# Kernel tuning notes

Hardware: AMD Instinct MI355X
Metric: run time of the kernel (lower is better)

Reference implementation:

```python
import jax, jax.numpy as jnp
import numpy as np

KERNEL_MUL = 2.0
KERNEL_NUM = 5
FIX_SIGMA = None


def setup_inputs() -> dict:
    key = jax.random.key(0)
    k1, k2 = jax.random.split(key)
    B, N, D = 4, 2048, 64
    return {
        "input": jax.random.normal(k1, (B, N, D), dtype=jnp.float32),
        "target": jax.random.normal(k2, (B, N, D), dtype=jnp.float32),
    }


def _mmd(x, y):
    B = x.shape[0]
    x = x.reshape(B, -1, x.shape[-1])
    y = y.reshape(B, -1, y.shape[-1])
    n = x.shape[1]
    total = jnp.concatenate([x, y], axis=1)          # [B, N, D], N = n + m
    N = total.shape[1]
    # pairwise squared L2 via |a|^2 + |b|^2 - 2 a.b (avoids [B,N,N,D] tensor)
    sq = jnp.sum(total * total, axis=-1)             # [B, N]
    gram = jnp.einsum('bnd,bmd->bnm', total, total)  # [B, N, N]
    L2 = sq[:, :, None] + sq[:, None, :] - 2.0 * gram
    if FIX_SIGMA is not None:
        bandwidth = jnp.full((B,), FIX_SIGMA, dtype=L2.dtype)
    else:
        bandwidth = jnp.sum(jax.lax.stop_gradient(L2), axis=(-1, -2)) / (N * N - N)
    bandwidth = bandwidth / (KERNEL_MUL ** (KERNEL_NUM // 2))   # [B]
    # multi-bandwidth Gaussian kernel sum (small fixed loop over KERNEL_NUM)
    kernels = jnp.zeros_like(L2)
    for i in range(KERNEL_NUM):
        bw_i = bandwidth * (KERNEL_MUL ** i)          # [B]
        kernels = kernels + jnp.exp(-L2 / bw_i[:, None, None])
    XX = kernels[:, :n, :n]
    YY = kernels[:, n:, n:]
    XY = kernels[:, :n, n:]
    YX = kernels[:, n:, :n]
    loss = (XX + YY - XY - YX).reshape(B, -1).mean(axis=-1)  # [B]
    return loss


def reference(input, target):
    return _mmd(input, target)
```

## Files before the change

kernel.cpp:

```cpp
#include <hip/hip_runtime.h>

#define N_TOT 4096
#define N_HALF 2048
#define DIMS 64
#define BATCH 4
#define WGRID 64
#define TRI_PER_BATCH 2080
#define NWG (BATCH * TRI_PER_BATCH)

typedef __attribute__((ext_vector_type(8))) short short8;
typedef __attribute__((ext_vector_type(4))) float f32x4;

#if __has_builtin(__builtin_amdgcn_exp2f)
#define EXP2F(x) __builtin_amdgcn_exp2f(x)
#else
#define EXP2F(x) exp2f(x)
#endif

__device__ __forceinline__ unsigned short f2bf_rne(float f) {
    unsigned int u = __float_as_uint(f);
    unsigned int r = (u + 0x7FFFu + ((u >> 16) & 1u)) >> 16;
    return (unsigned short)r;
}
__device__ __forceinline__ float bf2f(unsigned short h) {
    return __uint_as_float(((unsigned int)h) << 16);
}

__global__ __launch_bounds__(256) void prep_kernel(const float* __restrict__ x,
                                                   const float* __restrict__ y,
                                                   unsigned short* __restrict__ hi,
                                                   unsigned short* __restrict__ lo,
                                                   float* __restrict__ sq,
                                                   float* __restrict__ ssq_part,
                                                   float* __restrict__ colsum_part) {
    int g = blockIdx.x;
    int t = threadIdx.x;
    bool isx = g < 128;
    int gg = isx ? g : g - 128;
    int base = gg << 12;
    int b = gg >> 5;
    const float* src = isx ? x : y;

    float q_acc = 0.f;
    float4 c_acc = {0.f, 0.f, 0.f, 0.f};
#pragma unroll
    for (int it = 0; it < 4; ++it) {
        int e = base + (it << 10) + (t << 2);
        int rem = e & 131071;
        float4 v = *(const float4*)(src + e);
        unsigned dst = (unsigned)b * 262144u + (isx ? 0u : 131072u) + (unsigned)rem;
        ushort4 h, l;
        h.x = f2bf_rne(v.x); l.x = f2bf_rne(v.x - bf2f(h.x));
        h.y = f2bf_rne(v.y); l.y = f2bf_rne(v.y - bf2f(h.y));
        h.z = f2bf_rne(v.z); l.z = f2bf_rne(v.z - bf2f(h.z));
        h.w = f2bf_rne(v.w); l.w = f2bf_rne(v.w - bf2f(h.w));
        *(ushort4*)(hi + dst) = h;
        *(ushort4*)(lo + dst) = l;

        float p = fmaf(v.x, v.x, fmaf(v.y, v.y, fmaf(v.z, v.z, v.w * v.w)));
        p += __shfl_xor(p, 1);
        p += __shfl_xor(p, 2);
        p += __shfl_xor(p, 4);
        p += __shfl_xor(p, 8);
        int rwi = rem >> 6;
        if ((t & 15) == 0)
            sq[b * N_TOT + (isx ? rwi : N_HALF + rwi)] = p;

        float q = p;
        q += __shfl_xor(q, 16);
        q += __shfl_xor(q, 32);
        q_acc += q;

        float4 c = v;
        c.x += __shfl_xor(c.x, 16); c.y += __shfl_xor(c.y, 16);
        c.z += __shfl_xor(c.z, 16); c.w += __shfl_xor(c.w, 16);
        c.x += __shfl_xor(c.x, 32); c.y += __shfl_xor(c.y, 32);
        c.z += __shfl_xor(c.z, 32); c.w += __shfl_xor(c.w, 32);
        c_acc.x += c.x; c_acc.y += c.y; c_acc.z += c.z; c_acc.w += c.w;
    }

    __shared__ float wsum[4];
    __shared__ float4 csh[4][16];
    int wid = t >> 6;
    if ((t & 63) == 0) wsum[wid] = q_acc;
    if ((t & 63) < 16) csh[wid][t & 63] = c_acc;
    __syncthreads();
    if (t == 0) ssq_part[g] = wsum[0] + wsum[1] + wsum[2] + wsum[3];
    if (t < 16) {
        float4 s0 = csh[0][t], s1 = csh[1][t], s2 = csh[2][t], s3 = csh[3][t];
        float4 o;
        o.x = s0.x + s1.x + s2.x + s3.x;
        o.y = s0.y + s1.y + s2.y + s3.y;
        o.z = s0.z + s1.z + s2.z + s3.z;
        o.w = s0.w + s1.w + s2.w + s3.w;
        *(float4*)(colsum_part + (size_t)g * 64 + t * 4) = o;
    }
}

__global__ __launch_bounds__(256) void bw_kernel(const float* __restrict__ ssq_part,
                                                 const float* __restrict__ colsum_part,
                                                 float* __restrict__ k0arr) {
    int b = blockIdx.x;
    int t = threadIdx.x;
    int c = t & 63, q = t >> 6;
    float cs = 0.f;
#pragma unroll
    for (int pp = 0; pp < 16; ++pp) {
        int p = q * 16 + pp;
        int g = (p < 32) ? (b * 32 + p) : (128 + b * 32 + (p - 32));
        cs += colsum_part[(size_t)g * 64 + c];
    }
    __shared__ float csq[4][64];
    csq[q][c] = cs;
    __syncthreads();
    if (t < 64) {
        float col = csq[0][t] + csq[1][t] + csq[2][t] + csq[3][t];
        double cc = (double)col * (double)col;
#pragma unroll
        for (int o = 32; o > 0; o >>= 1) cc += __shfl_xor(cc, o);
        int g = (t < 32) ? (b * 32 + t) : (128 + b * 32 + (t - 32));
        double sd = (double)ssq_part[g];
#pragma unroll
        for (int o = 32; o > 0; o >>= 1) sd += __shfl_xor(sd, o);
        if (t == 0) {
            double sumL2 = 2.0 * (double)N_TOT * sd - 2.0 * cc;
            double bw = sumL2 / ((double)N_TOT * (double)N_TOT - (double)N_TOT);
            bw *= 0.25;
            k0arr[b] = (float)(-1.4426950408889634 / bw);
        }
    }
}

#define MMD_TILE_BODY(DIAGW)                                                   \
    _Pragma("unroll")                                                          \
    for (int mf = 0; mf < 4; ++mf) {                                           \
        unsigned ra = (i0 + (unsigned)mf * 16u + lrow) * 64u + kbase;          \
        short8 ah0 = *(const short8*)(Hb + ra);                                \
        short8 ah1 = *(const short8*)(Hb + ra + 32u);                          \
        short8 al0 = *(const short8*)(Lb + ra);                                \
        short8 al1 = *(const short8*)(Lb + ra + 32u);                          \
        float4 sv = *(const float4*)(sqb + i0 + (unsigned)mf * 16u + rquad);   \
        float ki0 = k16 * sv.x, ki1 = k16 * sv.y;                              \
        float ki2 = k16 * sv.z, ki3 = k16 * sv.w;                              \
        _Pragma("unroll")                                                      \
        for (int nf = 0; nf < 4; ++nf) {                                       \
            const short* bp = B0 + (nf * 16 + (int)lrow) * 8;                  \
            short8 bh0 = *(const short8*)(bp);                                 \
            short8 bh1 = *(const short8*)(bp + 2048);                          \
            f32x4 accP = (f32x4){0.f, 0.f, 0.f, 0.f};                          \
            f32x4 accQ = (f32x4){0.f, 0.f, 0.f, 0.f};                          \
            accP = __builtin_amdgcn_mfma_f32_16x16x32_bf16(ah0, bh0, accP, 0, 0, 0); \
            accQ = __builtin_amdgcn_mfma_f32_16x16x32_bf16(ah1, bh1, accQ, 0, 0, 0); \
            accP = __builtin_amdgcn_mfma_f32_16x16x32_bf16(al0, bh0, accP, 0, 0, 0); \
            accQ = __builtin_amdgcn_mfma_f32_16x16x32_bf16(al1, bh1, accQ, 0, 0, 0); \
            float kjn = (nf == 0) ? kj0 : (nf == 1) ? kj1 : (nf == 2) ? kj2 : kj3; \
            _Pragma("unroll")                                                  \
            for (int rg = 0; rg < 4; ++rg) {                                   \
                float kir = (rg == 0) ? ki0 : (rg == 1) ? ki1 : (rg == 2) ? ki2 : ki3; \
                float t16 = fmaf(m2k16, accQ[rg], fmaf(m2k16, accP[rg], kir + kjn)); \
                float e4 = EXP2F(t16);                                         \
                float e3 = e4 * e4;                                            \
                float e2 = e3 * e3;                                            \
                float e1 = e2 * e2;                                            \
                float e0 = e1 * e1;                                            \
                float es = ((e0 + e1) + (e2 + e3)) + e4;                       \
                if (DIAGW) {                                                   \
                    int i = mf * 16 + (int)rquad + rg;                         \
                    int j = nf * 16 + (int)lrow;                               \
                    float w = (j > i) ? 2.f : ((j == i) ? 1.f : 0.f);          \
                    es *= w;                                                   \
                }                                                              \
                if (rg & 1) eacc1 += es; else eacc0 += es;                     \
            }                                                                  \
        }                                                                      \
    }

__global__ void mmd_mfma(const unsigned short* __restrict__ hi,
                         const unsigned short* __restrict__ lo,
                         const float* __restrict__ sq,
                         const float* __restrict__ k0arr,
                         double* __restrict__ pblock) {
    int wg0 = blockIdx.x;
    int wg = (wg0 & 7) * (NWG / 8) + (wg0 >> 3);
    int b = wg / TRI_PER_BATCH;
    int r = wg % TRI_PER_BATCH;
    int ib = 0, cum = 0;
    while (r >= cum + (WGRID - ib)) { cum += WGRID - ib; ++ib; }
    int jb = ib + (r - cum);
    unsigned i0 = (unsigned)ib * 64u;
    unsigned j0 = (unsigned)jb * 64u;
    int lane = threadIdx.x;

    const unsigned short* Hb = hi + (unsigned)b * 262144u;
    const unsigned short* Lb = lo + (unsigned)b * 262144u;
    const float* sqb = sq + b * N_TOT;

    __shared__ short ldsB[4096];
    {
        unsigned gb = (j0 + (unsigned)lane) * 64u;
#pragma unroll
        for (int k = 0; k < 8; ++k) {
            short8 v = *(const short8*)(Hb + gb + (unsigned)k * 8u);
            *(short8*)(ldsB + k * 512 + lane * 8) = v;
        }
    }

    bool diag = (ib == jb);
    float wsign = ((i0 < (unsigned)N_HALF) == (j0 < (unsigned)N_HALF)) ? 1.f : -1.f;
    float k16 = k0arr[b] * 0.0625f;
    float m2k16 = -2.f * k16;
    unsigned lrow = (unsigned)(lane & 15);
    unsigned grp = (unsigned)(lane >> 4);
    unsigned rquad = grp * 4u;
    unsigned kbase = grp * 8u;

    float kj0 = k16 * sqb[j0 + 0u + lrow];
    float kj1 = k16 * sqb[j0 + 16u + lrow];
    float kj2 = k16 * sqb[j0 + 32u + lrow];
    float kj3 = k16 * sqb[j0 + 48u + lrow];

    const short* B0 = ldsB + grp * 512;
    float eacc0 = 0.f, eacc1 = 0.f;

    if (diag) {
        MMD_TILE_BODY(true)
    } else {
        MMD_TILE_BODY(false)
    }

    double acc_d = (double)((eacc0 + eacc1) * (diag ? wsign : 2.f * wsign));
#pragma unroll
    for (int o = 32; o > 0; o >>= 1) acc_d += __shfl_down(acc_d, o);
    if (lane == 0) pblock[wg] = acc_d;
}

__global__ __launch_bounds__(256) void finalize_kernel(const double* __restrict__ pblock,
                                                       float* __restrict__ out) {
    int b = blockIdx.x, t = threadIdx.x;
    const double* p = pblock + (size_t)b * TRI_PER_BATCH;
    double s = 0.0;
    for (int i = t; i < TRI_PER_BATCH; i += 256) s += p[i];
#pragma unroll
    for (int o = 32; o > 0; o >>= 1) s += __shfl_down(s, o);
    __shared__ double w[4];
    if ((t & 63) == 0) w[t >> 6] = s;
    __syncthreads();
    if (t == 0)
        out[b] = (float)((w[0] + w[1] + w[2] + w[3]) / ((double)N_HALF * (double)N_HALF));
}

extern "C" void kernel_launch(void* const* d_in, const int* in_sizes, int n_in,
                              void* d_out, int out_size, void* d_ws, size_t ws_size,
                              hipStream_t stream) {
    const float* x = (const float*)d_in[0];
    const float* y = (const float*)d_in[1];
    float* out = (float*)d_out;
    char* ws = (char*)d_ws;

    float*  k0arr       = (float*)ws;
    float*  ssq_part    = (float*)(ws + 4096);
    float*  colsum_part = (float*)(ws + 8192);
    double* pblock      = (double*)(ws + 8192);
    float*  sq          = (float*)(ws + 77824);
    unsigned short* tot_hi = (unsigned short*)(ws + 143360);
    unsigned short* tot_lo = (unsigned short*)(ws + 143360 + 2097152);

    prep_kernel<<<256, 256, 0, stream>>>(x, y, tot_hi, tot_lo, sq, ssq_part, colsum_part);
    bw_kernel<<<BATCH, 256, 0, stream>>>(ssq_part, colsum_part, k0arr);
    mmd_mfma<<<NWG, 64, 0, stream>>>(tot_hi, tot_lo, sq, k0arr, pblock);
    finalize_kernel<<<BATCH, 256, 0, stream>>>(pblock, out);
}
```

Baseline: 45.25 us.

## Process two column tiles per workgroup to reuse row-tile A fragments

Each workgroup now handles a pair of adjacent 64x64 upper-triangular tiles in the same row block, so the A-side hi/lo fragments and row norms loaded from global memory are reused across two B tiles. This halves the number of workgroups and roughly halves the A-load traffic per tile. The cost is twice the LDS per workgroup, more live registers and fewer workgroups to hide latency. An odd trailing tile is covered by a duplicated, zero-weighted second tile, which wastes some compute.

```diff
diff --git a/kernel.cpp b/kernel.cpp
--- a/kernel.cpp
+++ b/kernel.cpp
@@ -6,7 +6,8 @@
 #define BATCH 4
 #define WGRID 64
 #define TRI_PER_BATCH 2080
-#define NWG (BATCH * TRI_PER_BATCH)
+#define NJOB_PER_BATCH 1056
+#define NJOB (BATCH * NJOB_PER_BATCH)
 
 typedef __attribute__((ext_vector_type(8))) short short8;
 typedef __attribute__((ext_vector_type(4))) float f32x4;
@@ -131,7 +132,7 @@
     }
 }
 
-#define MMD_TILE_BODY(DIAGW)                                                   \
+#define MMD_PAIR_BODY(DIAGA)                                                   \
     _Pragma("unroll")                                                          \
     for (int mf = 0; mf < 4; ++mf) {                                           \
         unsigned ra = (i0 + (unsigned)mf * 16u + lrow) * 64u + kbase;          \
@@ -144,7 +145,7 @@
         float ki2 = k16 * sv.z, ki3 = k16 * sv.w;                              \
         _Pragma("unroll")                                                      \
         for (int nf = 0; nf < 4; ++nf) {                                       \
-            const short* bp = B0 + (nf * 16 + (int)lrow) * 8;                  \
+            const short* bp = B0A + (nf * 16 + (int)lrow) * 8;                 \
             short8 bh0 = *(const short8*)(bp);                                 \
             short8 bh1 = *(const short8*)(bp + 2048);                          \
             f32x4 accP = (f32x4){0.f, 0.f, 0.f, 0.f};                          \
@@ -153,7 +154,7 @@
             accQ = __builtin_amdgcn_mfma_f32_16x16x32_bf16(ah1, bh1, accQ, 0, 0, 0); \
             accP = __builtin_amdgcn_mfma_f32_16x16x32_bf16(al0, bh0, accP, 0, 0, 0); \
             accQ = __builtin_amdgcn_mfma_f32_16x16x32_bf16(al1, bh1, accQ, 0, 0, 0); \
-            float kjn = (nf == 0) ? kj0 : (nf == 1) ? kj1 : (nf == 2) ? kj2 : kj3; \
+            float kjn = (nf == 0) ? kjA0 : (nf == 1) ? kjA1 : (nf == 2) ? kjA2 : kjA3; \
             _Pragma("unroll")                                                  \
             for (int rg = 0; rg < 4; ++rg) {                                   \
                 float kir = (rg == 0) ? ki0 : (rg == 1) ? ki1 : (rg == 2) ? ki2 : ki3; \
@@ -164,13 +165,38 @@
                 float e1 = e2 * e2;                                            \
                 float e0 = e1 * e1;                                            \
                 float es = ((e0 + e1) + (e2 + e3)) + e4;                       \
-                if (DIAGW) {                                                   \
+                if (DIAGA) {                                                   \
                     int i = mf * 16 + (int)rquad + rg;                         \
                     int j = nf * 16 + (int)lrow;                               \
                     float w = (j > i) ? 2.f : ((j == i) ? 1.f : 0.f);          \
                     es *= w;                                                   \
                 }                                                              \
-                if (rg & 1) eacc1 += es; else eacc0 += es;                     \
+                if (rg & 1) eaccA1 += es; else eaccA0 += es;                   \
+            }                                                                  \
+        }                                                                      \
+        _Pragma("unroll")                                                      \
+        for (int nf = 0; nf < 4; ++nf) {                                       \
+            const short* bp = B0B + (nf * 16 + (int)lrow) * 8;                 \
+            short8 bh0 = *(const short8*)(bp);                                 \
+            short8 bh1 = *(const short8*)(bp + 2048);                          \
+            f32x4 accP = (f32x4){0.f, 0.f, 0.f, 0.f};                          \
+            f32x4 accQ = (f32x4){0.f, 0.f, 0.f, 0.f};                          \
+            accP = __builtin_amdgcn_mfma_f32_16x16x32_bf16(ah0, bh0, accP, 0, 0, 0); \
+            accQ = __builtin_amdgcn_mfma_f32_16x16x32_bf16(ah1, bh1, accQ, 0, 0, 0); \
+            accP = __builtin_amdgcn_mfma_f32_16x16x32_bf16(al0, bh0, accP, 0, 0, 0); \
+            accQ = __builtin_amdgcn_mfma_f32_16x16x32_bf16(al1, bh1, accQ, 0, 0, 0); \
+            float kjn = (nf == 0) ? kjB0 : (nf == 1) ? kjB1 : (nf == 2) ? kjB2 : kjB3; \
+            _Pragma("unroll")                                                  \
+            for (int rg = 0; rg < 4; ++rg) {                                   \
+                float kir = (rg == 0) ? ki0 : (rg == 1) ? ki1 : (rg == 2) ? ki2 : ki3; \
+                float t16 = fmaf(m2k16, accQ[rg], fmaf(m2k16, accP[rg], kir + kjn)); \
+                float e4 = EXP2F(t16);                                         \
+                float e3 = e4 * e4;                                            \
+                float e2 = e3 * e3;                                            \
+                float e1 = e2 * e2;                                            \
+                float e0 = e1 * e1;                                            \
+                float es = ((e0 + e1) + (e2 + e3)) + e4;                       \
+                if (rg & 1) eaccB1 += es; else eaccB0 += es;                   \
             }                                                                  \
         }                                                                      \
     }
@@ -181,32 +207,43 @@
                          const float* __restrict__ k0arr,
                          double* __restrict__ pblock) {
     int wg0 = blockIdx.x;
-    int wg = (wg0 & 7) * (NWG / 8) + (wg0 >> 3);
-    int b = wg / TRI_PER_BATCH;
-    int r = wg % TRI_PER_BATCH;
+    int job = (wg0 & 7) * (NJOB / 8) + (wg0 >> 3);
+    int b = job / NJOB_PER_BATCH;
+    int r = job % NJOB_PER_BATCH;
     int ib = 0, cum = 0;
-    while (r >= cum + (WGRID - ib)) { cum += WGRID - ib; ++ib; }
-    int jb = ib + (r - cum);
+    while (r >= cum + ((65 - ib) >> 1)) { cum += (65 - ib) >> 1; ++ib; }
+    int k = r - cum;
+    int jbA = ib + 2 * k;
+    bool has2 = (ib + 2 * k + 1) < WGRID;
+    int jbB = has2 ? (jbA + 1) : jbA;
     unsigned i0 = (unsigned)ib * 64u;
-    unsigned j0 = (unsigned)jb * 64u;
+    unsigned j0A = (unsigned)jbA * 64u;
+    unsigned j0B = (unsigned)jbB * 64u;
     int lane = threadIdx.x;
 
     const unsigned short* Hb = hi + (unsigned)b * 262144u;
     const unsigned short* Lb = lo + (unsigned)b * 262144u;
     const float* sqb = sq + b * N_TOT;
 
-    __shared__ short ldsB[4096];
+    __shared__ short ldsB[8192];
     {
-        unsigned gb = (j0 + (unsigned)lane) * 64u;
-#pragma unroll
-        for (int k = 0; k < 8; ++k) {
-            short8 v = *(const short8*)(Hb + gb + (unsigned)k * 8u);
-            *(short8*)(ldsB + k * 512 + lane * 8) = v;
+        unsigned gbA = (j0A + (unsigned)lane) * 64u;
+        unsigned gbB = (j0B + (unsigned)lane) * 64u;
+#pragma unroll
+        for (int kk = 0; kk < 8; ++kk) {
+            short8 vA = *(const short8*)(Hb + gbA + (unsigned)kk * 8u);
+            short8 vB = *(const short8*)(Hb + gbB + (unsigned)kk * 8u);
+            *(short8*)(ldsB + kk * 512 + lane * 8) = vA;
+            *(short8*)(ldsB + 4096 + kk * 512 + lane * 8) = vB;
         }
     }
 
-    bool diag = (ib == jb);
-    float wsign = ((i0 < (unsigned)N_HALF) == (j0 < (unsigned)N_HALF)) ? 1.f : -1.f;
+    bool diagA = (k == 0);
+    float wsignA = ((i0 < (unsigned)N_HALF) == (j0A < (unsigned)N_HALF)) ? 1.f : -1.f;
+    float wsignB = ((i0 < (unsigned)N_HALF) == (j0B < (unsigned)N_HALF)) ? 1.f : -1.f;
+    float scaleA = diagA ? wsignA : 2.f * wsignA;
+    float scaleB = has2 ? 2.f * wsignB : 0.f;
+
     float k16 = k0arr[b] * 0.0625f;
     float m2k16 = -2.f * k16;
     unsigned lrow = (unsigned)(lane & 15);
@@ -214,32 +251,38 @@
     unsigned rquad = grp * 4u;
     unsigned kbase = grp * 8u;
 
-    float kj0 = k16 * sqb[j0 + 0u + lrow];
-    float kj1 = k16 * sqb[j0 + 16u + lrow];
-    float kj2 = k16 * sqb[j0 + 32u + lrow];
-    float kj3 = k16 * sqb[j0 + 48u + lrow];
-
-    const short* B0 = ldsB + grp * 512;
-    float eacc0 = 0.f, eacc1 = 0.f;
-
-    if (diag) {
-        MMD_TILE_BODY(true)
+    float kjA0 = k16 * sqb[j0A + 0u + lrow];
+    float kjA1 = k16 * sqb[j0A + 16u + lrow];
+    float kjA2 = k16 * sqb[j0A + 32u + lrow];
+    float kjA3 = k16 * sqb[j0A + 48u + lrow];
+    float kjB0 = k16 * sqb[j0B + 0u + lrow];
+    float kjB1 = k16 * sqb[j0B + 16u + lrow];
+    float kjB2 = k16 * sqb[j0B + 32u + lrow];
+    float kjB3 = k16 * sqb[j0B + 48u + lrow];
+
+    const short* B0A = ldsB + grp * 512;
+    const short* B0B = ldsB + 4096 + grp * 512;
+    float eaccA0 = 0.f, eaccA1 = 0.f, eaccB0 = 0.f, eaccB1 = 0.f;
+
+    if (diagA) {
+        MMD_PAIR_BODY(true)
     } else {
-        MMD_TILE_BODY(false)
-    }
-
-    double acc_d = (double)((eacc0 + eacc1) * (diag ? wsign : 2.f * wsign));
+        MMD_PAIR_BODY(false)
+    }
+
+    double acc_d = (double)((eaccA0 + eaccA1) * scaleA) +
+                   (double)((eaccB0 + eaccB1) * scaleB);
 #pragma unroll
     for (int o = 32; o > 0; o >>= 1) acc_d += __shfl_down(acc_d, o);
-    if (lane == 0) pblock[wg] = acc_d;
+    if (lane == 0) pblock[job] = acc_d;
 }
 
 __global__ __launch_bounds__(256) void finalize_kernel(const double* __restrict__ pblock,
                                                        float* __restrict__ out) {
     int b = blockIdx.x, t = threadIdx.x;
-    const double* p = pblock + (size_t)b * TRI_PER_BATCH;
+    const double* p = pblock + (size_t)b * NJOB_PER_BATCH;
     double s = 0.0;
-    for (int i = t; i < TRI_PER_BATCH; i += 256) s += p[i];
+    for (int i = t; i < NJOB_PER_BATCH; i += 256) s += p[i];
 #pragma unroll
     for (int o = 32; o > 0; o >>= 1) s += __shfl_down(s, o);
     __shared__ double w[4];
@@ -267,6 +310,6 @@
 
     prep_kernel<<<256, 256, 0, stream>>>(x, y, tot_hi, tot_lo, sq, ssq_part, colsum_part);
     bw_kernel<<<BATCH, 256, 0, stream>>>(ssq_part, colsum_part, k0arr);
-    mmd_mfma<<<NWG, 64, 0, stream>>>(tot_hi, tot_lo, sq, k0arr, pblock);
+    mmd_mfma<<<NJOB, 64, 0, stream>>>(tot_hi, tot_lo, sq, k0arr, pblock);
     finalize_kernel<<<BATCH, 256, 0, stream>>>(pblock, out);
 }
```

New measurement: 74.19 us. 63.9% more time.
